# Kernel tuning notes

Hardware: AMD Instinct MI355X
Metric: run time of the kernel (lower is better)

The kernel has to match this reference:

```python
import jax, jax.numpy as jnp
import numpy as np

BINS = 256
H = 2048
N = 2_000_000


def _tensor2image(x):
    # standard GAN denorm: [-1,1] -> [0,1]
    return (x + 1.0) * 0.5


def _cdf(vals):
    # torch.histc(bins=256, min=0, max=256): unit-width bins, values in [0,255]
    idx = jnp.clip(jnp.floor(vals), 0, BINS - 1).astype(jnp.int32)
    hist = jnp.zeros((BINS,), jnp.float32).at[idx].add(1.0)
    return jnp.cumsum(hist) / hist.sum()


def _trans_table(ref_cdf, adj_cdf):
    # cal_trans: for i in 1..255, first j in 1..255 with adj[j-1] <= ref[i] <= adj[j]
    i_vals = ref_cdf[1:]  # [255]
    cond = (adj_cdf[:-1][None, :] <= i_vals[:, None]) & (i_vals[:, None] <= adj_cdf[1:][None, :])  # [255,255]
    found = cond.any(axis=1)
    first_j = jnp.argmax(cond, axis=1) + 1
    tab = jnp.where(found, first_j, jnp.arange(1, BINS))  # unmatched entries keep identity
    tab = jnp.concatenate([jnp.zeros((1,), tab.dtype), tab])
    tab = tab.at[BINS - 1].set(BINS - 1)
    return tab.astype(jnp.float32)


def _hist_match(dst_img, ref_img, i0, i1, i2, i3):
    # dst_img, ref_img: [3,H,W]; indices: [N]
    dst_align = dst_img[:, i0, i1]  # [3,N]
    ref_align = ref_img[:, i2, i3]  # [3,N]
    cdf_dst = jax.vmap(_cdf)(dst_align)  # [3,256]
    cdf_ref = jax.vmap(_cdf)(ref_align)  # [3,256]
    tables = jax.vmap(_trans_table)(cdf_dst, cdf_ref)  # [3,256]
    bins = jnp.clip(dst_align, 0, BINS - 1).astype(jnp.int32)  # int() truncation on [0,255]
    new_align = jnp.take_along_axis(tables, bins, axis=1)  # [3,N]
    return dst_img.at[:, i0, i1].set(new_align)


def reference(input_data, target_data, mask_src, mask_tar, index0, index1, index2, index3, ref_data):
    inp = _tensor2image(input_data) * 255.0
    tgt = _tensor2image(target_data) * 255.0
    ref = _tensor2image(ref_data) * 255.0
    h = mask_src.shape[2]
    m_src = jnp.broadcast_to(mask_src, (1, 3, h, h))
    m_tar = jnp.broadcast_to(mask_tar, (1, 3, h, h))
    input_masked = inp * m_src
    target_masked = (tgt * m_tar)[0]  # [3,H,W]
    ref_masked = (ref * m_src)[0]     # [3,H,W]
    i0, i1, i2, i3 = index0[0], index1[0], index2[0], index3[0]
    matched = _hist_match(ref_masked, target_masked, i0, i1, i2, i3)[None]  # [1,3,H,W]
    input_match = jax.lax.stop_gradient(matched) * m_src  # no_grad in original
    return jnp.mean((input_masked - input_match) ** 2)


def setup_inputs() -> dict:
    key = jax.random.key(0)
    ks = jax.random.split(key, 9)
    inp = {
        "input_data": jax.random.uniform(ks[0], (1, 3, H, H), jnp.float32, -1.0, 1.0),
        "target_data": jax.random.uniform(ks[1], (1, 3, H, H), jnp.float32, -1.0, 1.0),
        "mask_src": (jax.random.uniform(ks[2], (1, 1, H, H)) > 0.5).astype(jnp.float32),
        "mask_tar": (jax.random.uniform(ks[3], (1, 1, H, H)) > 0.5).astype(jnp.float32),
        "index0": jax.random.randint(ks[4], (1, N), 0, H, jnp.int32),
        "index1": jax.random.randint(ks[5], (1, N), 0, H, jnp.int32),
        "index2": jax.random.randint(ks[6], (1, N), 0, H, jnp.int32),
        "index3": jax.random.randint(ks[7], (1, N), 0, H, jnp.int32),
        "ref_data": jax.random.uniform(ks[8], (1, 3, H, H), jnp.float32, -1.0, 1.0),
    }
    return inp
```

## Files before the change

kernel.cpp:

```cpp
#include <hip/hip_runtime.h>

#define HDIM 2048
#define HH (HDIM * HDIM)
#define NIDX 2000000
#define BINS 256
#define NCOPY 16

#define ACC_OFF      0
#define HIST_OFF     256
#define TAB_OFF      102400
#define BITS_OFF     131072
#define PACKED_D_OFF 1048576
#define PACKED_R_OFF 17825792
#define WS_ZERO_BYTES (BITS_OFF + HH / 8)

__global__ __launch_bounds__(256) void pack_kernel(
    const float* __restrict__ ref, const float* __restrict__ tgt,
    const float* __restrict__ msrc, const float* __restrict__ mtar,
    unsigned* __restrict__ packed_d, unsigned* __restrict__ packed_r)
{
    const int stride = gridDim.x * 256;
    for (int g = blockIdx.x * 256 + threadIdx.x; g < HH / 4; g += stride) {
        const int p = g * 4;
        const float4 ms4 = *(const float4*)(msrc + p);
        const float4 mt4 = *(const float4*)(mtar + p);
        const float ms[4] = {ms4.x, ms4.y, ms4.z, ms4.w};
        const float mt[4] = {mt4.x, mt4.y, mt4.z, mt4.w};
        unsigned od[4] = {0, 0, 0, 0}, orr[4] = {0, 0, 0, 0};
#pragma unroll
        for (int c = 0; c < 3; c++) {
            const float4 rv = *(const float4*)(ref + c * HH + p);
            const float4 tv = *(const float4*)(tgt + c * HH + p);
            const float r[4] = {rv.x, rv.y, rv.z, rv.w};
            const float t[4] = {tv.x, tv.y, tv.z, tv.w};
#pragma unroll
            for (int k = 0; k < 4; k++) {
                const float vd = ((r[k] + 1.0f) * 0.5f) * 255.0f * ms[k];
                const float vr = ((t[k] + 1.0f) * 0.5f) * 255.0f * mt[k];
                const unsigned bd = (unsigned)(int)fminf(fmaxf(floorf(vd), 0.0f), 255.0f);
                const unsigned br = (unsigned)(int)fminf(fmaxf(floorf(vr), 0.0f), 255.0f);
                od[k]  |= bd << (8 * c);
                orr[k] |= br << (8 * c);
            }
        }
        *(uint4*)(packed_d + p) = make_uint4(od[0], od[1], od[2], od[3]);
        *(uint4*)(packed_r + p) = make_uint4(orr[0], orr[1], orr[2], orr[3]);
    }
}

__global__ __launch_bounds__(256) void hist_kernel(
    const unsigned* __restrict__ packed_d, const unsigned* __restrict__ packed_r,
    const int* __restrict__ i0, const int* __restrict__ i1,
    const int* __restrict__ i2, const int* __restrict__ i3,
    unsigned* __restrict__ hist, unsigned* __restrict__ bits)
{
    __shared__ unsigned lhist[6 * BINS];
    for (int t = threadIdx.x; t < 6 * BINS; t += 256) lhist[t] = 0;
    __syncthreads();

    const int stride = gridDim.x * 256;
    for (int n2 = blockIdx.x * 256 + threadIdx.x; n2 < NIDX / 2; n2 += stride) {
        const int2 a = *(const int2*)(i0 + 2 * n2);
        const int2 b = *(const int2*)(i1 + 2 * n2);
        const int2 c = *(const int2*)(i2 + 2 * n2);
        const int2 d = *(const int2*)(i3 + 2 * n2);
        const int pd0 = a.x * HDIM + b.x, pd1 = a.y * HDIM + b.y;
        const int pr0 = c.x * HDIM + d.x, pr1 = c.y * HDIM + d.y;
        const unsigned wd0 = packed_d[pd0];
        const unsigned wd1 = packed_d[pd1];
        const unsigned wr0 = packed_r[pr0];
        const unsigned wr1 = packed_r[pr1];
        atomicOr(&bits[pd0 >> 5], 1u << (pd0 & 31));
        atomicOr(&bits[pd1 >> 5], 1u << (pd1 & 31));
        atomicAdd(&lhist[              (wd0       & 255u)], 1u);
        atomicAdd(&lhist[1 * BINS + ((wd0 >> 8)  & 255u)], 1u);
        atomicAdd(&lhist[2 * BINS + ((wd0 >> 16) & 255u)], 1u);
        atomicAdd(&lhist[              (wd1       & 255u)], 1u);
        atomicAdd(&lhist[1 * BINS + ((wd1 >> 8)  & 255u)], 1u);
        atomicAdd(&lhist[2 * BINS + ((wd1 >> 16) & 255u)], 1u);
        atomicAdd(&lhist[3 * BINS + ((wr0)       & 255u)], 1u);
        atomicAdd(&lhist[4 * BINS + ((wr0 >> 8)  & 255u)], 1u);
        atomicAdd(&lhist[5 * BINS + ((wr0 >> 16) & 255u)], 1u);
        atomicAdd(&lhist[3 * BINS + ((wr1)       & 255u)], 1u);
        atomicAdd(&lhist[4 * BINS + ((wr1 >> 8)  & 255u)], 1u);
        atomicAdd(&lhist[5 * BINS + ((wr1 >> 16) & 255u)], 1u);
    }
    __syncthreads();
    unsigned* h = hist + (blockIdx.x & (NCOPY - 1)) * (6 * BINS);
    for (int t = threadIdx.x; t < 6 * BINS; t += 256) {
        const unsigned v = lhist[t];
        if (v) atomicAdd(&h[t], v);
    }
}

__global__ __launch_bounds__(256) void table_kernel(
    const unsigned* __restrict__ hist, float* __restrict__ tables)
{
    __shared__ float cdf_d[3][BINS];
    __shared__ float cdf_r[3][BINS];
    __shared__ unsigned wsum[4];
    const int t = threadIdx.x;
    const int lane = t & 63;
    const int wid = t >> 6;

    for (int ch = 0; ch < 6; ch++) {
        unsigned x = 0;
#pragma unroll
        for (int cp = 0; cp < NCOPY; cp++) x += hist[cp * (6 * BINS) + ch * BINS + t];
#pragma unroll
        for (int d = 1; d < 64; d <<= 1) {
            const unsigned y = __shfl_up(x, d, 64);
            if (lane >= d) x += y;
        }
        if (lane == 63) wsum[wid] = x;
        __syncthreads();
        unsigned prefix = 0;
        for (int w = 0; w < wid; w++) prefix += wsum[w];
        x += prefix;
        const float f = (float)x / 2000000.0f;
        if (ch < 3) cdf_d[ch][t] = f;
        else        cdf_r[ch - 3][t] = f;
        __syncthreads();
    }

    for (int c = 0; c < 3; c++) {
        float out;
        if (t == 0)             out = 0.0f;
        else if (t == BINS - 1) out = 255.0f;
        else {
            const float v = cdf_d[c][t];
            const float* arr = cdf_r[c];
            int lo = 0, hi = 256;
            while (lo < hi) { const int mid = (lo + hi) >> 1; if (arr[mid] < v) lo = mid + 1; else hi = mid; }
            const int J0 = ((lo > 1) ? lo : 1) - 1;
            int lo2 = 0, hi2 = 256;
            while (lo2 < hi2) { const int mid = (lo2 + hi2) >> 1; if (arr[mid] <= v) lo2 = mid + 1; else hi2 = mid; }
            const int J1 = ((lo2 - 1) < 254 ? (lo2 - 1) : 254);
            const bool found = (lo2 >= 1) && (J0 <= J1);
            out = found ? (float)(J0 + 1) : (float)t;
        }
        tables[c * BINS + t] = out;
    }
}

__global__ __launch_bounds__(256) void loss_kernel(
    const float* __restrict__ inp, const float* __restrict__ ref,
    const float* __restrict__ msrc, const float* __restrict__ tables_g,
    const unsigned* __restrict__ bits, double* __restrict__ acc)
{
    __shared__ float tab[3 * BINS];
    for (int t = threadIdx.x; t < 3 * BINS; t += 256) tab[t] = tables_g[t];
    __syncthreads();

    double local = 0.0;
    const int ngroups = 3 * HH / 4;
    const int stride = gridDim.x * 256;
    for (int g = blockIdx.x * 256 + threadIdx.x; g < ngroups; g += stride) {
        const int c = g / (HH / 4);
        const int p = (g - c * (HH / 4)) * 4;
        const float4 rv = *(const float4*)(ref + c * HH + p);
        const float4 iv = *(const float4*)(inp + c * HH + p);
        const float4 mv = *(const float4*)(msrc + p);
        const unsigned w = bits[p >> 5] >> (p & 31);
        const float r[4] = {rv.x, rv.y, rv.z, rv.w};
        const float x[4] = {iv.x, iv.y, iv.z, iv.w};
        const float m[4] = {mv.x, mv.y, mv.z, mv.w};
        float s = 0.0f;
#pragma unroll
        for (int k = 0; k < 4; k++) {
            const float mm = m[k];
            const float refm = ((r[k] + 1.0f) * 0.5f) * 255.0f * mm;
            const float inpm = ((x[k] + 1.0f) * 0.5f) * 255.0f * mm;
            float matchv;
            if ((w >> k) & 1u) {
                const int bidx = (int)fminf(fmaxf(refm, 0.0f), 255.0f);
                matchv = tab[c * BINS + bidx];
            } else {
                matchv = refm;
            }
            const float d = inpm - matchv * mm;
            s += d * d;
        }
        local += (double)s;
    }

    __shared__ double red[256];
    red[threadIdx.x] = local;
    __syncthreads();
    for (int s2 = 128; s2 > 0; s2 >>= 1) {
        if (threadIdx.x < s2) red[threadIdx.x] += red[threadIdx.x + s2];
        __syncthreads();
    }
    if (threadIdx.x == 0) atomicAdd(acc, red[0]);
}

__global__ void finalize_kernel(const double* __restrict__ acc, float* __restrict__ out)
{
    out[0] = (float)(acc[0] / (double)(3 * HH));
}

extern "C" void kernel_launch(void* const* d_in, const int* in_sizes, int n_in,
                              void* d_out, int out_size, void* d_ws, size_t ws_size,
                              hipStream_t stream)
{
    const float* input_data  = (const float*)d_in[0];
    const float* target_data = (const float*)d_in[1];
    const float* mask_src    = (const float*)d_in[2];
    const float* mask_tar    = (const float*)d_in[3];
    const int*   i0          = (const int*)d_in[4];
    const int*   i1          = (const int*)d_in[5];
    const int*   i2          = (const int*)d_in[6];
    const int*   i3          = (const int*)d_in[7];
    const float* ref_data    = (const float*)d_in[8];
    float* out = (float*)d_out;

    char* ws = (char*)d_ws;
    double*   acc      = (double*)(ws + ACC_OFF);
    unsigned* hist     = (unsigned*)(ws + HIST_OFF);
    float*    tables   = (float*)(ws + TAB_OFF);
    unsigned* bits     = (unsigned*)(ws + BITS_OFF);
    unsigned* packed_d = (unsigned*)(ws + PACKED_D_OFF);
    unsigned* packed_r = (unsigned*)(ws + PACKED_R_OFF);

    hipMemsetAsync(ws, 0, WS_ZERO_BYTES, stream);
    pack_kernel<<<2048, 256, 0, stream>>>(ref_data, target_data, mask_src, mask_tar,
                                          packed_d, packed_r);
    hist_kernel<<<2048, 256, 0, stream>>>(packed_d, packed_r, i0, i1, i2, i3, hist, bits);
    table_kernel<<<1, 256, 0, stream>>>(hist, tables);
    loss_kernel<<<4096, 256, 0, stream>>>(input_data, ref_data, mask_src, tables, bits, acc);
    finalize_kernel<<<1, 1, 0, stream>>>(acc, out);
}
```

Before: 372.0 us.

## Count index hits in packed top byte and build histograms from per-pixel counts

The per-index gather plus shared-atomic histogram and separate visited bitmap are replaced by a scatter kernel. It does global atomicAdd of a hit count into the unused top byte of each packed pixel word. A dense combine kernel then streams the packed arrays and adds weighted counts into shared histograms, and the loss kernel reads the visited flag and precomputed bins from the packed word, processing all three channels per pixel. The final atomic double add is replaced by per-block partials reduced in a finalize kernel. This adds a full 16M-pixel streaming pass and risks 8-bit count overflow if a pixel is hit 256 or more times, though that is unlikely with random indices.

```diff
diff --git a/kernel.cpp b/kernel.cpp
--- a/kernel.cpp
+++ b/kernel.cpp
@@ -5,14 +5,14 @@
 #define NIDX 2000000
 #define BINS 256
 #define NCOPY 16
-
-#define ACC_OFF      0
-#define HIST_OFF     256
-#define TAB_OFF      102400
-#define BITS_OFF     131072
+#define LOSS_BLOCKS 1024
+
+#define PART_OFF     0
+#define HIST_OFF     8192
+#define TAB_OFF      106496
 #define PACKED_D_OFF 1048576
 #define PACKED_R_OFF 17825792
-#define WS_ZERO_BYTES (BITS_OFF + HH / 8)
+#define WS_ZERO_BYTES (TAB_OFF + 3072)
 
 __global__ __launch_bounds__(256) void pack_kernel(
     const float* __restrict__ ref, const float* __restrict__ tgt,
@@ -48,42 +48,76 @@
     }
 }
 
-__global__ __launch_bounds__(256) void hist_kernel(
-    const unsigned* __restrict__ packed_d, const unsigned* __restrict__ packed_r,
+__global__ __launch_bounds__(256) void scatter_kernel(
     const int* __restrict__ i0, const int* __restrict__ i1,
     const int* __restrict__ i2, const int* __restrict__ i3,
-    unsigned* __restrict__ hist, unsigned* __restrict__ bits)
+    unsigned* __restrict__ packed_d, unsigned* __restrict__ packed_r)
+{
+    const int stride = gridDim.x * 256;
+    for (int q = blockIdx.x * 256 + threadIdx.x; q < NIDX / 4; q += stride) {
+        const int4 a = ((const int4*)i0)[q];
+        const int4 b = ((const int4*)i1)[q];
+        const int4 c = ((const int4*)i2)[q];
+        const int4 d = ((const int4*)i3)[q];
+        atomicAdd(&packed_d[a.x * HDIM + b.x], 1u << 24);
+        atomicAdd(&packed_d[a.y * HDIM + b.y], 1u << 24);
+        atomicAdd(&packed_d[a.z * HDIM + b.z], 1u << 24);
+        atomicAdd(&packed_d[a.w * HDIM + b.w], 1u << 24);
+        atomicAdd(&packed_r[c.x * HDIM + d.x], 1u << 24);
+        atomicAdd(&packed_r[c.y * HDIM + d.y], 1u << 24);
+        atomicAdd(&packed_r[c.z * HDIM + d.z], 1u << 24);
+        atomicAdd(&packed_r[c.w * HDIM + d.w], 1u << 24);
+    }
+}
+
+__global__ __launch_bounds__(256) void combine_kernel(
+    const unsigned* __restrict__ packed_d, const unsigned* __restrict__ packed_r,
+    unsigned* __restrict__ hist)
 {
     __shared__ unsigned lhist[6 * BINS];
     for (int t = threadIdx.x; t < 6 * BINS; t += 256) lhist[t] = 0;
     __syncthreads();
 
-    const int stride = gridDim.x * 256;
-    for (int n2 = blockIdx.x * 256 + threadIdx.x; n2 < NIDX / 2; n2 += stride) {
-        const int2 a = *(const int2*)(i0 + 2 * n2);
-        const int2 b = *(const int2*)(i1 + 2 * n2);
-        const int2 c = *(const int2*)(i2 + 2 * n2);
-        const int2 d = *(const int2*)(i3 + 2 * n2);
-        const int pd0 = a.x * HDIM + b.x, pd1 = a.y * HDIM + b.y;
-        const int pr0 = c.x * HDIM + d.x, pr1 = c.y * HDIM + d.y;
-        const unsigned wd0 = packed_d[pd0];
-        const unsigned wd1 = packed_d[pd1];
-        const unsigned wr0 = packed_r[pr0];
-        const unsigned wr1 = packed_r[pr1];
-        atomicOr(&bits[pd0 >> 5], 1u << (pd0 & 31));
-        atomicOr(&bits[pd1 >> 5], 1u << (pd1 & 31));
-        atomicAdd(&lhist[              (wd0       & 255u)], 1u);
-        atomicAdd(&lhist[1 * BINS + ((wd0 >> 8)  & 255u)], 1u);
-        atomicAdd(&lhist[2 * BINS + ((wd0 >> 16) & 255u)], 1u);
-        atomicAdd(&lhist[              (wd1       & 255u)], 1u);
-        atomicAdd(&lhist[1 * BINS + ((wd1 >> 8)  & 255u)], 1u);
-        atomicAdd(&lhist[2 * BINS + ((wd1 >> 16) & 255u)], 1u);
-        atomicAdd(&lhist[3 * BINS + ((wr0)       & 255u)], 1u);
-        atomicAdd(&lhist[4 * BINS + ((wr0 >> 8)  & 255u)], 1u);
-        atomicAdd(&lhist[5 * BINS + ((wr0 >> 16) & 255u)], 1u);
-        atomicAdd(&lhist[3 * BINS + ((wr1)       & 255u)], 1u);
-        atomicAdd(&lhist[4 * BINS + ((wr1 >> 8)  & 255u)], 1u);
-        atomicAdd(&lhist[5 * BINS + ((wr1 >> 16) & 255u)], 1u);
+    unsigned b0d = 0, b0r = 0;
+    const int stride = gridDim.x * 256;
+    for (int g = blockIdx.x * 256 + threadIdx.x; g < HH / 4; g += stride) {
+        const uint4 wd4 = ((const uint4*)packed_d)[g];
+        const uint4 wr4 = ((const uint4*)packed_r)[g];
+        const unsigned wd[4] = {wd4.x, wd4.y, wd4.z, wd4.w};
+        const unsigned wr[4] = {wr4.x, wr4.y, wr4.z, wr4.w};
+#pragma unroll
+        for (int k = 0; k < 4; k++) {
+            const unsigned cd = wd[k] >> 24;
+            if (cd) {
+                const unsigned bins = wd[k] & 0xFFFFFFu;
+                if (bins == 0) b0d += cd;
+                else {
+                    atomicAdd(&lhist[           (bins        & 255u)], cd);
+                    atomicAdd(&lhist[1 * BINS + ((bins >> 8)  & 255u)], cd);
+                    atomicAdd(&lhist[2 * BINS + ((bins >> 16) & 255u)], cd);
+                }
+            }
+            const unsigned cr = wr[k] >> 24;
+            if (cr) {
+                const unsigned bins = wr[k] & 0xFFFFFFu;
+                if (bins == 0) b0r += cr;
+                else {
+                    atomicAdd(&lhist[3 * BINS + (bins        & 255u)], cr);
+                    atomicAdd(&lhist[4 * BINS + ((bins >> 8)  & 255u)], cr);
+                    atomicAdd(&lhist[5 * BINS + ((bins >> 16) & 255u)], cr);
+                }
+            }
+        }
+    }
+    if (b0d) {
+        atomicAdd(&lhist[0 * BINS], b0d);
+        atomicAdd(&lhist[1 * BINS], b0d);
+        atomicAdd(&lhist[2 * BINS], b0d);
+    }
+    if (b0r) {
+        atomicAdd(&lhist[3 * BINS], b0r);
+        atomicAdd(&lhist[4 * BINS], b0r);
+        atomicAdd(&lhist[5 * BINS], b0r);
     }
     __syncthreads();
     unsigned* h = hist + (blockIdx.x & (NCOPY - 1)) * (6 * BINS);
@@ -146,42 +180,43 @@
 __global__ __launch_bounds__(256) void loss_kernel(
     const float* __restrict__ inp, const float* __restrict__ ref,
     const float* __restrict__ msrc, const float* __restrict__ tables_g,
-    const unsigned* __restrict__ bits, double* __restrict__ acc)
+    const unsigned* __restrict__ packed_d, double* __restrict__ partials)
 {
     __shared__ float tab[3 * BINS];
     for (int t = threadIdx.x; t < 3 * BINS; t += 256) tab[t] = tables_g[t];
     __syncthreads();
 
     double local = 0.0;
-    const int ngroups = 3 * HH / 4;
-    const int stride = gridDim.x * 256;
-    for (int g = blockIdx.x * 256 + threadIdx.x; g < ngroups; g += stride) {
-        const int c = g / (HH / 4);
-        const int p = (g - c * (HH / 4)) * 4;
-        const float4 rv = *(const float4*)(ref + c * HH + p);
-        const float4 iv = *(const float4*)(inp + c * HH + p);
+    const int stride = gridDim.x * 256;
+    for (int g = blockIdx.x * 256 + threadIdx.x; g < HH / 4; g += stride) {
+        const int p = g * 4;
         const float4 mv = *(const float4*)(msrc + p);
-        const unsigned w = bits[p >> 5] >> (p & 31);
-        const float r[4] = {rv.x, rv.y, rv.z, rv.w};
-        const float x[4] = {iv.x, iv.y, iv.z, iv.w};
+        const uint4 pk4 = *(const uint4*)(packed_d + p);
         const float m[4] = {mv.x, mv.y, mv.z, mv.w};
-        float s = 0.0f;
-#pragma unroll
-        for (int k = 0; k < 4; k++) {
-            const float mm = m[k];
-            const float refm = ((r[k] + 1.0f) * 0.5f) * 255.0f * mm;
-            const float inpm = ((x[k] + 1.0f) * 0.5f) * 255.0f * mm;
-            float matchv;
-            if ((w >> k) & 1u) {
-                const int bidx = (int)fminf(fmaxf(refm, 0.0f), 255.0f);
-                matchv = tab[c * BINS + bidx];
-            } else {
-                matchv = refm;
-            }
-            const float d = inpm - matchv * mm;
-            s += d * d;
-        }
-        local += (double)s;
+        const unsigned pw[4] = {pk4.x, pk4.y, pk4.z, pk4.w};
+#pragma unroll
+        for (int c = 0; c < 3; c++) {
+            const float4 rv = *(const float4*)(ref + c * HH + p);
+            const float4 iv = *(const float4*)(inp + c * HH + p);
+            const float r[4] = {rv.x, rv.y, rv.z, rv.w};
+            const float x[4] = {iv.x, iv.y, iv.z, iv.w};
+            float s = 0.0f;
+#pragma unroll
+            for (int k = 0; k < 4; k++) {
+                const float mm = m[k];
+                const float refm = ((r[k] + 1.0f) * 0.5f) * 255.0f * mm;
+                const float inpm = ((x[k] + 1.0f) * 0.5f) * 255.0f * mm;
+                float matchv;
+                if (pw[k] >> 24) {
+                    matchv = tab[c * BINS + ((pw[k] >> (8 * c)) & 255u)];
+                } else {
+                    matchv = refm;
+                }
+                const float d = inpm - matchv * mm;
+                s += d * d;
+            }
+            local += (double)s;
+        }
     }
 
     __shared__ double red[256];
@@ -191,12 +226,22 @@
         if (threadIdx.x < s2) red[threadIdx.x] += red[threadIdx.x + s2];
         __syncthreads();
     }
-    if (threadIdx.x == 0) atomicAdd(acc, red[0]);
-}
-
-__global__ void finalize_kernel(const double* __restrict__ acc, float* __restrict__ out)
-{
-    out[0] = (float)(acc[0] / (double)(3 * HH));
+    if (threadIdx.x == 0) partials[blockIdx.x] = red[0];
+}
+
+__global__ __launch_bounds__(256) void finalize_kernel(
+    const double* __restrict__ partials, float* __restrict__ out)
+{
+    const int t = threadIdx.x;
+    double s = partials[t] + partials[t + 256] + partials[t + 512] + partials[t + 768];
+    __shared__ double red[256];
+    red[t] = s;
+    __syncthreads();
+    for (int s2 = 128; s2 > 0; s2 >>= 1) {
+        if (t < s2) red[t] += red[t + s2];
+        __syncthreads();
+    }
+    if (t == 0) out[0] = (float)(red[0] / (double)(3 * HH));
 }
 
 extern "C" void kernel_launch(void* const* d_in, const int* in_sizes, int n_in,
@@ -215,18 +260,19 @@
     float* out = (float*)d_out;
 
     char* ws = (char*)d_ws;
-    double*   acc      = (double*)(ws + ACC_OFF);
+    double*   partials = (double*)(ws + PART_OFF);
     unsigned* hist     = (unsigned*)(ws + HIST_OFF);
     float*    tables   = (float*)(ws + TAB_OFF);
-    unsigned* bits     = (unsigned*)(ws + BITS_OFF);
     unsigned* packed_d = (unsigned*)(ws + PACKED_D_OFF);
     unsigned* packed_r = (unsigned*)(ws + PACKED_R_OFF);
 
     hipMemsetAsync(ws, 0, WS_ZERO_BYTES, stream);
     pack_kernel<<<2048, 256, 0, stream>>>(ref_data, target_data, mask_src, mask_tar,
                                           packed_d, packed_r);
-    hist_kernel<<<2048, 256, 0, stream>>>(packed_d, packed_r, i0, i1, i2, i3, hist, bits);
+    scatter_kernel<<<2048, 256, 0, stream>>>(i0, i1, i2, i3, packed_d, packed_r);
+    combine_kernel<<<2048, 256, 0, stream>>>(packed_d, packed_r, hist);
     table_kernel<<<1, 256, 0, stream>>>(hist, tables);
-    loss_kernel<<<4096, 256, 0, stream>>>(input_data, ref_data, mask_src, tables, bits, acc);
-    finalize_kernel<<<1, 1, 0, stream>>>(acc, out);
-}
+    loss_kernel<<<LOSS_BLOCKS, 256, 0, stream>>>(input_data, ref_data, mask_src, tables,
+                                                 packed_d, partials);
+    finalize_kernel<<<1, 256, 0, stream>>>(partials, out);
+}
```

Result: slower. 422.6 us (+13.6%).

## Fuse table build into loss kernel and drop memset and finalize launches

Applied to the files above, without the earlier changes.

Zeroing of the histogram, bitmask and counter moves into pack_kernel, so the separate memset goes away. Every block of the new tabloss kernel recomputes the 256-bin CDF and lookup tables in shared memory, which replaces the single-block table kernel and its launch. The final reduction uses per-block partial sums and a last-block-done counter instead of a finalize kernel. The hist kernel now reads indices as int4, and the loss loop processes all three channels per pixel so the mask and bitmask words are reused. The cost is redundant table computation in each of the 2048 blocks, plus a threadfence and counter atomic per block.

```diff
diff --git a/kernel.cpp b/kernel.cpp
--- a/kernel.cpp
+++ b/kernel.cpp
@@ -5,22 +5,30 @@
 #define NIDX 2000000
 #define BINS 256
 #define NCOPY 16
-
-#define ACC_OFF      0
-#define HIST_OFF     256
-#define TAB_OFF      102400
+#define TL_BLOCKS 2048
+
+#define PART_OFF     0
+#define CNT_OFF      16384
+#define HIST_OFF     20480
 #define BITS_OFF     131072
 #define PACKED_D_OFF 1048576
 #define PACKED_R_OFF 17825792
-#define WS_ZERO_BYTES (BITS_OFF + HH / 8)
 
 __global__ __launch_bounds__(256) void pack_kernel(
     const float* __restrict__ ref, const float* __restrict__ tgt,
     const float* __restrict__ msrc, const float* __restrict__ mtar,
-    unsigned* __restrict__ packed_d, unsigned* __restrict__ packed_r)
-{
+    unsigned* __restrict__ packed_d, unsigned* __restrict__ packed_r,
+    unsigned* __restrict__ hist, unsigned* __restrict__ bits,
+    unsigned* __restrict__ counter)
+{
+    const int gtid = blockIdx.x * 256 + threadIdx.x;
     const int stride = gridDim.x * 256;
-    for (int g = blockIdx.x * 256 + threadIdx.x; g < HH / 4; g += stride) {
+
+    if (gtid == 0) *counter = 0;
+    for (int k = gtid; k < NCOPY * 6 * BINS; k += stride) hist[k] = 0;
+    for (int k = gtid; k < HH / 32; k += stride) bits[k] = 0;
+
+    for (int g = gtid; g < HH / 4; g += stride) {
         const int p = g * 4;
         const float4 ms4 = *(const float4*)(msrc + p);
         const float4 mt4 = *(const float4*)(mtar + p);
@@ -32,11 +40,11 @@
             const float4 rv = *(const float4*)(ref + c * HH + p);
             const float4 tv = *(const float4*)(tgt + c * HH + p);
             const float r[4] = {rv.x, rv.y, rv.z, rv.w};
-            const float t[4] = {tv.x, tv.y, tv.z, tv.w};
+            const float tt[4] = {tv.x, tv.y, tv.z, tv.w};
 #pragma unroll
             for (int k = 0; k < 4; k++) {
                 const float vd = ((r[k] + 1.0f) * 0.5f) * 255.0f * ms[k];
-                const float vr = ((t[k] + 1.0f) * 0.5f) * 255.0f * mt[k];
+                const float vr = ((tt[k] + 1.0f) * 0.5f) * 255.0f * mt[k];
                 const unsigned bd = (unsigned)(int)fminf(fmaxf(floorf(vd), 0.0f), 255.0f);
                 const unsigned br = (unsigned)(int)fminf(fmaxf(floorf(vr), 0.0f), 255.0f);
                 od[k]  |= bd << (8 * c);
@@ -55,53 +63,57 @@
     unsigned* __restrict__ hist, unsigned* __restrict__ bits)
 {
     __shared__ unsigned lhist[6 * BINS];
-    for (int t = threadIdx.x; t < 6 * BINS; t += 256) lhist[t] = 0;
+    for (int k = threadIdx.x; k < 6 * BINS; k += 256) lhist[k] = 0;
     __syncthreads();
 
     const int stride = gridDim.x * 256;
-    for (int n2 = blockIdx.x * 256 + threadIdx.x; n2 < NIDX / 2; n2 += stride) {
-        const int2 a = *(const int2*)(i0 + 2 * n2);
-        const int2 b = *(const int2*)(i1 + 2 * n2);
-        const int2 c = *(const int2*)(i2 + 2 * n2);
-        const int2 d = *(const int2*)(i3 + 2 * n2);
-        const int pd0 = a.x * HDIM + b.x, pd1 = a.y * HDIM + b.y;
-        const int pr0 = c.x * HDIM + d.x, pr1 = c.y * HDIM + d.y;
-        const unsigned wd0 = packed_d[pd0];
-        const unsigned wd1 = packed_d[pd1];
-        const unsigned wr0 = packed_r[pr0];
-        const unsigned wr1 = packed_r[pr1];
-        atomicOr(&bits[pd0 >> 5], 1u << (pd0 & 31));
-        atomicOr(&bits[pd1 >> 5], 1u << (pd1 & 31));
-        atomicAdd(&lhist[              (wd0       & 255u)], 1u);
-        atomicAdd(&lhist[1 * BINS + ((wd0 >> 8)  & 255u)], 1u);
-        atomicAdd(&lhist[2 * BINS + ((wd0 >> 16) & 255u)], 1u);
-        atomicAdd(&lhist[              (wd1       & 255u)], 1u);
-        atomicAdd(&lhist[1 * BINS + ((wd1 >> 8)  & 255u)], 1u);
-        atomicAdd(&lhist[2 * BINS + ((wd1 >> 16) & 255u)], 1u);
-        atomicAdd(&lhist[3 * BINS + ((wr0)       & 255u)], 1u);
-        atomicAdd(&lhist[4 * BINS + ((wr0 >> 8)  & 255u)], 1u);
-        atomicAdd(&lhist[5 * BINS + ((wr0 >> 16) & 255u)], 1u);
-        atomicAdd(&lhist[3 * BINS + ((wr1)       & 255u)], 1u);
-        atomicAdd(&lhist[4 * BINS + ((wr1 >> 8)  & 255u)], 1u);
-        atomicAdd(&lhist[5 * BINS + ((wr1 >> 16) & 255u)], 1u);
+    for (int q = blockIdx.x * 256 + threadIdx.x; q < NIDX / 4; q += stride) {
+        const int4 a = ((const int4*)i0)[q];
+        const int4 b = ((const int4*)i1)[q];
+        const int4 c = ((const int4*)i2)[q];
+        const int4 d = ((const int4*)i3)[q];
+        const int pd[4] = {a.x * HDIM + b.x, a.y * HDIM + b.y, a.z * HDIM + b.z, a.w * HDIM + b.w};
+        const int pr[4] = {c.x * HDIM + d.x, c.y * HDIM + d.y, c.z * HDIM + d.z, c.w * HDIM + d.w};
+        unsigned wd[4], wr[4];
+#pragma unroll
+        for (int k = 0; k < 4; k++) wd[k] = packed_d[pd[k]];
+#pragma unroll
+        for (int k = 0; k < 4; k++) wr[k] = packed_r[pr[k]];
+#pragma unroll
+        for (int k = 0; k < 4; k++) atomicOr(&bits[pd[k] >> 5], 1u << (pd[k] & 31));
+#pragma unroll
+        for (int k = 0; k < 4; k++) {
+            atomicAdd(&lhist[           ( wd[k]        & 255u)], 1u);
+            atomicAdd(&lhist[1 * BINS + ((wd[k] >> 8 ) & 255u)], 1u);
+            atomicAdd(&lhist[2 * BINS + ((wd[k] >> 16) & 255u)], 1u);
+            atomicAdd(&lhist[3 * BINS + ( wr[k]        & 255u)], 1u);
+            atomicAdd(&lhist[4 * BINS + ((wr[k] >> 8 ) & 255u)], 1u);
+            atomicAdd(&lhist[5 * BINS + ((wr[k] >> 16) & 255u)], 1u);
+        }
     }
     __syncthreads();
     unsigned* h = hist + (blockIdx.x & (NCOPY - 1)) * (6 * BINS);
-    for (int t = threadIdx.x; t < 6 * BINS; t += 256) {
-        const unsigned v = lhist[t];
-        if (v) atomicAdd(&h[t], v);
-    }
-}
-
-__global__ __launch_bounds__(256) void table_kernel(
-    const unsigned* __restrict__ hist, float* __restrict__ tables)
-{
-    __shared__ float cdf_d[3][BINS];
-    __shared__ float cdf_r[3][BINS];
+    for (int k = threadIdx.x; k < 6 * BINS; k += 256) {
+        const unsigned v = lhist[k];
+        if (v) atomicAdd(&h[k], v);
+    }
+}
+
+__global__ __launch_bounds__(256) void tabloss_kernel(
+    const float* __restrict__ inp, const float* __restrict__ ref,
+    const float* __restrict__ msrc, const unsigned* __restrict__ hist,
+    const unsigned* __restrict__ bits, double* __restrict__ partials,
+    unsigned* __restrict__ counter, float* __restrict__ out)
+{
+    __shared__ float    cdf[6 * BINS];
+    __shared__ float    tab[3 * BINS];
+    __shared__ double   red[256];
     __shared__ unsigned wsum[4];
-    const int t = threadIdx.x;
+    __shared__ unsigned is_last;
+
+    const int t    = threadIdx.x;
     const int lane = t & 63;
-    const int wid = t >> 6;
+    const int wid  = t >> 6;
 
     for (int ch = 0; ch < 6; ch++) {
         unsigned x = 0;
@@ -117,19 +129,16 @@
         unsigned prefix = 0;
         for (int w = 0; w < wid; w++) prefix += wsum[w];
         x += prefix;
-        const float f = (float)x / 2000000.0f;
-        if (ch < 3) cdf_d[ch][t] = f;
-        else        cdf_r[ch - 3][t] = f;
-        __syncthreads();
-    }
-
+        cdf[ch * BINS + t] = (float)x / 2000000.0f;
+        __syncthreads();
+    }
     for (int c = 0; c < 3; c++) {
-        float out;
-        if (t == 0)             out = 0.0f;
-        else if (t == BINS - 1) out = 255.0f;
+        float o;
+        if (t == 0)             o = 0.0f;
+        else if (t == BINS - 1) o = 255.0f;
         else {
-            const float v = cdf_d[c][t];
-            const float* arr = cdf_r[c];
+            const float v = cdf[c * BINS + t];
+            const float* arr = cdf + (3 + c) * BINS;
             int lo = 0, hi = 256;
             while (lo < hi) { const int mid = (lo + hi) >> 1; if (arr[mid] < v) lo = mid + 1; else hi = mid; }
             const int J0 = ((lo > 1) ? lo : 1) - 1;
@@ -137,66 +146,70 @@
             while (lo2 < hi2) { const int mid = (lo2 + hi2) >> 1; if (arr[mid] <= v) lo2 = mid + 1; else hi2 = mid; }
             const int J1 = ((lo2 - 1) < 254 ? (lo2 - 1) : 254);
             const bool found = (lo2 >= 1) && (J0 <= J1);
-            out = found ? (float)(J0 + 1) : (float)t;
-        }
-        tables[c * BINS + t] = out;
-    }
-}
-
-__global__ __launch_bounds__(256) void loss_kernel(
-    const float* __restrict__ inp, const float* __restrict__ ref,
-    const float* __restrict__ msrc, const float* __restrict__ tables_g,
-    const unsigned* __restrict__ bits, double* __restrict__ acc)
-{
-    __shared__ float tab[3 * BINS];
-    for (int t = threadIdx.x; t < 3 * BINS; t += 256) tab[t] = tables_g[t];
+            o = found ? (float)(J0 + 1) : (float)t;
+        }
+        tab[c * BINS + t] = o;
+    }
     __syncthreads();
 
     double local = 0.0;
-    const int ngroups = 3 * HH / 4;
     const int stride = gridDim.x * 256;
-    for (int g = blockIdx.x * 256 + threadIdx.x; g < ngroups; g += stride) {
-        const int c = g / (HH / 4);
-        const int p = (g - c * (HH / 4)) * 4;
-        const float4 rv = *(const float4*)(ref + c * HH + p);
-        const float4 iv = *(const float4*)(inp + c * HH + p);
+    for (int g = blockIdx.x * 256 + t; g < HH / 4; g += stride) {
+        const int p = g * 4;
         const float4 mv = *(const float4*)(msrc + p);
         const unsigned w = bits[p >> 5] >> (p & 31);
-        const float r[4] = {rv.x, rv.y, rv.z, rv.w};
-        const float x[4] = {iv.x, iv.y, iv.z, iv.w};
         const float m[4] = {mv.x, mv.y, mv.z, mv.w};
-        float s = 0.0f;
-#pragma unroll
-        for (int k = 0; k < 4; k++) {
-            const float mm = m[k];
-            const float refm = ((r[k] + 1.0f) * 0.5f) * 255.0f * mm;
-            const float inpm = ((x[k] + 1.0f) * 0.5f) * 255.0f * mm;
-            float matchv;
-            if ((w >> k) & 1u) {
-                const int bidx = (int)fminf(fmaxf(refm, 0.0f), 255.0f);
-                matchv = tab[c * BINS + bidx];
-            } else {
-                matchv = refm;
+#pragma unroll
+        for (int c = 0; c < 3; c++) {
+            const float4 rv = *(const float4*)(ref + c * HH + p);
+            const float4 iv = *(const float4*)(inp + c * HH + p);
+            const float r[4] = {rv.x, rv.y, rv.z, rv.w};
+            const float x4[4] = {iv.x, iv.y, iv.z, iv.w};
+            float s = 0.0f;
+#pragma unroll
+            for (int k = 0; k < 4; k++) {
+                const float mm = m[k];
+                const float refm = ((r[k] + 1.0f) * 0.5f) * 255.0f * mm;
+                const float inpm = ((x4[k] + 1.0f) * 0.5f) * 255.0f * mm;
+                float matchv;
+                if ((w >> k) & 1u) {
+                    const int bidx = (int)fminf(fmaxf(refm, 0.0f), 255.0f);
+                    matchv = tab[c * BINS + bidx];
+                } else {
+                    matchv = refm;
+                }
+                const float dd = inpm - matchv * mm;
+                s += dd * dd;
             }
-            const float d = inpm - matchv * mm;
-            s += d * d;
-        }
-        local += (double)s;
-    }
-
-    __shared__ double red[256];
-    red[threadIdx.x] = local;
+            local += (double)s;
+        }
+    }
+    red[t] = local;
     __syncthreads();
     for (int s2 = 128; s2 > 0; s2 >>= 1) {
-        if (threadIdx.x < s2) red[threadIdx.x] += red[threadIdx.x + s2];
-        __syncthreads();
-    }
-    if (threadIdx.x == 0) atomicAdd(acc, red[0]);
-}
-
-__global__ void finalize_kernel(const double* __restrict__ acc, float* __restrict__ out)
-{
-    out[0] = (float)(acc[0] / (double)(3 * HH));
+        if (t < s2) red[t] += red[t + s2];
+        __syncthreads();
+    }
+    if (t == 0) partials[blockIdx.x] = red[0];
+
+    __threadfence();
+    if (t == 0) {
+        const unsigned prev = atomicAdd(counter, 1u);
+        is_last = (prev == (unsigned)(gridDim.x - 1)) ? 1u : 0u;
+    }
+    __syncthreads();
+    if (is_last) {
+        double s = 0.0;
+        for (int k = t; k < TL_BLOCKS; k += 256)
+            s += __hip_atomic_load(&partials[k], __ATOMIC_RELAXED, __HIP_MEMORY_SCOPE_AGENT);
+        red[t] = s;
+        __syncthreads();
+        for (int s2 = 128; s2 > 0; s2 >>= 1) {
+            if (t < s2) red[t] += red[t + s2];
+            __syncthreads();
+        }
+        if (t == 0) out[0] = (float)(red[0] / (double)(3 * HH));
+    }
 }
 
 extern "C" void kernel_launch(void* const* d_in, const int* in_sizes, int n_in,
@@ -215,18 +228,16 @@
     float* out = (float*)d_out;
 
     char* ws = (char*)d_ws;
-    double*   acc      = (double*)(ws + ACC_OFF);
+    double*   partials = (double*)(ws + PART_OFF);
+    unsigned* counter  = (unsigned*)(ws + CNT_OFF);
     unsigned* hist     = (unsigned*)(ws + HIST_OFF);
-    float*    tables   = (float*)(ws + TAB_OFF);
     unsigned* bits     = (unsigned*)(ws + BITS_OFF);
     unsigned* packed_d = (unsigned*)(ws + PACKED_D_OFF);
     unsigned* packed_r = (unsigned*)(ws + PACKED_R_OFF);
 
-    hipMemsetAsync(ws, 0, WS_ZERO_BYTES, stream);
     pack_kernel<<<2048, 256, 0, stream>>>(ref_data, target_data, mask_src, mask_tar,
-                                          packed_d, packed_r);
+                                          packed_d, packed_r, hist, bits, counter);
     hist_kernel<<<2048, 256, 0, stream>>>(packed_d, packed_r, i0, i1, i2, i3, hist, bits);
-    table_kernel<<<1, 256, 0, stream>>>(hist, tables);
-    loss_kernel<<<4096, 256, 0, stream>>>(input_data, ref_data, mask_src, tables, bits, acc);
-    finalize_kernel<<<1, 1, 0, stream>>>(acc, out);
-}
+    tabloss_kernel<<<TL_BLOCKS, 256, 0, stream>>>(input_data, ref_data, mask_src, hist,
+                                                  bits, partials, counter, out);
+}
```

Measured after the change: 553.6 us. +48.8%, slower.
